# Kernel tuning notes

Hardware: AMD Instinct MI355X
Metric: run time of the kernel (lower is better)

## Reference

```python
import jax, jax.numpy as jnp
import numpy as np

TEMPERATURE = 0.07
EPS = 1e-12  # matches F.normalize eps clamp


def setup_inputs() -> dict:
    key = jax.random.key(0)
    k1, k2 = jax.random.split(key)
    B, S, D = 8, 512, 128
    return {
        "z_i": jax.random.normal(k1, (B, S, D), dtype=jnp.float32),
        "z_j": jax.random.normal(k2, (B, S, D), dtype=jnp.float32),
    }


def reference(z_i, z_j):
    D = z_i.shape[-1]
    zi = z_i.reshape(-1, D)  # [N, D]
    zj = z_j.reshape(-1, D)
    # cosine normalization (use_cosine_similarity=True)
    zi = zi / jnp.maximum(jnp.linalg.norm(zi, axis=1, keepdims=True), EPS)
    zj = zj / jnp.maximum(jnp.linalg.norm(zj, axis=1, keepdims=True), EPS)
    N = zi.shape[0]
    z = jnp.concatenate([zi, zj], axis=0)  # [2N, D]
    sim = (z @ z.T) / TEMPERATURE  # [2N, 2N]
    # denominator: logsumexp over all j != i (positives + negatives)
    diag = jnp.eye(2 * N, dtype=bool)
    lse = jax.nn.logsumexp(jnp.where(diag, -jnp.inf, sim), axis=1)  # [2N]
    # positive logit for row i is sim[i, (i+N) mod 2N] = <zi, zj>/T for both halves
    pos_half = jnp.sum(zi * zj, axis=1) / TEMPERATURE  # [N]
    pos = jnp.concatenate([pos_half, pos_half])  # [2N]
    return jnp.mean(-pos + lse)
```

## Files before the change

### kernel.cpp

```cpp
#include <hip/hip_runtime.h>
#include <stdint.h>


#define TOTAL   8192
#define NHALF   4096
#define DK      128
#define TEMP_INV 14.285714285714286f
#define SCALE    4.539816f

#define TILE    128
#define TILES   (TOTAL / TILE)
#define NBLK    (TILES * (TILES + 1) / 2)
#define BN      64
#define NSTAGE  (TILE / BN)

typedef short  bf16x8  __attribute__((ext_vector_type(8)));
typedef float  floatx4 __attribute__((ext_vector_type(4)));

#if __has_builtin(__builtin_amdgcn_exp2f)
#define EXP2(x) __builtin_amdgcn_exp2f(x)
#else
#define EXP2(x) exp2f(x)
#endif

__device__ __forceinline__ uint32_t f2bf(float f) {
  uint32_t u = __float_as_uint(f);
  return (u + 0x7fffu + ((u >> 16) & 1u)) >> 16;
}
__device__ __forceinline__ uint32_t pack2bf(float lo, float hi) {
  return f2bf(lo) | (f2bf(hi) << 16);
}

__global__ __launch_bounds__(256) void ntx_norm(
    const float* __restrict__ zi, const float* __restrict__ zj,
    uint32_t* __restrict__ zn,
    float* __restrict__ pos,
    float* __restrict__ rowsum)
{
  const int t = threadIdx.x;
  if (blockIdx.x < 32) rowsum[blockIdx.x * 256 + t] = 0.0f;

  const int wave = t >> 6, lane = t & 63;
  const int i = blockIdx.x * 4 + wave;

  const float2 vi = *(const float2*)(zi + (size_t)i * DK + lane * 2);
  const float2 vj = *(const float2*)(zj + (size_t)i * DK + lane * 2);
  float ssi = vi.x * vi.x + vi.y * vi.y;
  float ssj = vj.x * vj.x + vj.y * vj.y;
  float dij = vi.x * vj.x + vi.y * vj.y;
#pragma unroll
  for (int m = 1; m <= 32; m <<= 1) {
    ssi += __shfl_xor(ssi, m, 64);
    ssj += __shfl_xor(ssj, m, 64);
    dij += __shfl_xor(dij, m, 64);
  }
  const float invi = 1.0f / fmaxf(sqrtf(ssi), 1e-12f);
  const float invj = 1.0f / fmaxf(sqrtf(ssj), 1e-12f);

  zn[(size_t)i * 64 + lane] =
      pack2bf(vi.x * invi * SCALE, vi.y * invi * SCALE);
  zn[(size_t)(i + NHALF) * 64 + lane] =
      pack2bf(vj.x * invj * SCALE, vj.y * invj * SCALE);
  if (lane == 0) pos[i] = dij * invi * invj * TEMP_INV;
}

__global__ __launch_bounds__(128, 3) void ntx_gemm(
    const uint16_t* __restrict__ z,
    float* __restrict__ rowsum)
{
  __shared__ uint4 lb4[BN * 17];
  __shared__ float colacc[2][TILE];

  int I = 0, rem = (int)blockIdx.x, span = TILES;
  while (rem >= span) { rem -= span; --span; ++I; }
  const int J = I + rem;
  const bool isdiag = (I == J);

  const int t = threadIdx.x;
  const int wave = t >> 6, lane = t & 63;
  const int q = lane >> 4, c = lane & 15;
  const int i0 = I * TILE;
  const int j0 = J * TILE;
  const int rowbase = i0 + wave * 64;

  bf16x8 afrag[4][4];
#pragma unroll
  for (int s = 0; s < 4; ++s) {
    const uint16_t* ap = z + (size_t)(rowbase + s * 16 + c) * DK + q * 8;
#pragma unroll
    for (int kk = 0; kk < 4; ++kk)
      afrag[s][kk] = *(const bf16x8*)(ap + kk * 32);
  }

  float runsum[4][4];
#pragma unroll
  for (int s = 0; s < 4; ++s)
#pragma unroll
    for (int r = 0; r < 4; ++r) runsum[s][r] = 0.0f;

  const int ch = t & 15;
  const int r0 = t >> 4;

  for (int st = 0; st < NSTAGE; ++st) {
    const int jst = j0 + st * BN;
    __syncthreads();
#pragma unroll
    for (int p = 0; p < 8; ++p) {
      const int r = r0 + p * 8;
      uint4 v = *(const uint4*)(z + (size_t)(jst + r) * DK + ch * 8);
      lb4[r * 17 + ch] = v;
    }
    __syncthreads();

#pragma unroll
    for (int jt = 0; jt < BN / 16; ++jt) {
      bf16x8 bfrag[4];
#pragma unroll
      for (int kk = 0; kk < 4; ++kk)
        bfrag[kk] = *(const bf16x8*)&lb4[(jt * 16 + c) * 17 + kk * 4 + q];
      const int jc = jst + jt * 16;

      float colv = 0.0f;
#pragma unroll
      for (int s = 0; s < 4; ++s) {
        floatx4 acc = {0.0f, 0.0f, 0.0f, 0.0f};
#pragma unroll
        for (int kk = 0; kk < 4; ++kk)
          acc = __builtin_amdgcn_mfma_f32_16x16x32_bf16(afrag[s][kk],
                                                        bfrag[kk], acc,
                                                        0, 0, 0);
        const int rb = rowbase + s * 16;
        if (!isdiag) {
#pragma unroll
          for (int r = 0; r < 4; ++r) {
            float e = EXP2(acc[r]);
            runsum[s][r] += e;
            colv += e;
          }
        } else if (jc == rb) {
#pragma unroll
          for (int r = 0; r < 4; ++r) {
            float e = EXP2(acc[r]);
            runsum[s][r] += (q * 4 + r == c) ? 0.0f : e;
          }
        } else {
#pragma unroll
          for (int r = 0; r < 4; ++r) runsum[s][r] += EXP2(acc[r]);
        }
      }

      if (!isdiag) {
        colv += __shfl_xor(colv, 16, 64);
        colv += __shfl_xor(colv, 32, 64);
        if (lane < 16)
          colacc[wave][st * BN + jt * 16 + lane] = colv;
      }
    }
  }

#pragma unroll
  for (int s = 0; s < 4; ++s)
#pragma unroll
    for (int r = 0; r < 4; ++r) {
      float v = runsum[s][r];
      v += __shfl_xor(v, 1, 64);
      v += __shfl_xor(v, 2, 64);
      v += __shfl_xor(v, 4, 64);
      v += __shfl_xor(v, 8, 64);
      runsum[s][r] = v;
    }
  if (c == 0) {
#pragma unroll
    for (int s = 0; s < 4; ++s)
#pragma unroll
      for (int r = 0; r < 4; ++r)
        atomicAdd(&rowsum[rowbase + s * 16 + q * 4 + r], runsum[s][r]);
  }

  __syncthreads();
  if (!isdiag && t < TILE)
    atomicAdd(&rowsum[j0 + t], colacc[0][t] + colacc[1][t]);
}

__global__ __launch_bounds__(1024) void ntx_final(
    const float* __restrict__ rowsum, const float* __restrict__ pos,
    float* __restrict__ out)
{
  const int t = threadIdx.x;
  float acc = 0.0f;
  for (int r = t; r < TOTAL; r += 1024) acc += __logf(rowsum[r]);
  for (int r = t; r < NHALF; r += 1024) acc -= 2.0f * pos[r];
#pragma unroll
  for (int m = 1; m <= 32; m <<= 1) acc += __shfl_xor(acc, m, 64);
  __shared__ float red[16];
  const int wave = t >> 6, lane = t & 63;
  if (lane == 0) red[wave] = acc;
  __syncthreads();
  if (t == 0) {
    float s = 0.0f;
#pragma unroll
    for (int w = 0; w < 16; ++w) s += red[w];
    out[0] = s / (float)TOTAL;
  }
}

extern "C" void kernel_launch(void* const* d_in, const int* in_sizes, int n_in,
                              void* d_out, int out_size, void* d_ws,
                              size_t ws_size, hipStream_t stream) {
  const float* zi = (const float*)d_in[0];
  const float* zj = (const float*)d_in[1];
  float* out = (float*)d_out;

  char* ws = (char*)d_ws;
  uint16_t* zn     = (uint16_t*)ws;
  float*    rowsum = (float*)(ws + (size_t)TOTAL * DK * 2);
  float*    pos    = (float*)(ws + (size_t)TOTAL * DK * 2 + TOTAL * 4);

  ntx_norm<<<dim3(NHALF / 4), dim3(256), 0, stream>>>(zi, zj, (uint32_t*)zn,
                                                      pos, rowsum);
  ntx_gemm<<<dim3(NBLK), dim3(128), 0, stream>>>(zn, rowsum);
  ntx_final<<<dim3(1), dim3(1024), 0, stream>>>(rowsum, pos, out);
}
```

Measured before the change: 100.9 us.

## Use 4-wave GEMM blocks and replace atomics with deterministic per-block scratch reduction

```diff
diff --git a/kernel.cpp b/kernel.cpp
--- a/kernel.cpp
+++ b/kernel.cpp
@@ -34,12 +34,9 @@
 __global__ __launch_bounds__(256) void ntx_norm(
     const float* __restrict__ zi, const float* __restrict__ zj,
     uint32_t* __restrict__ zn,
-    float* __restrict__ pos,
-    float* __restrict__ rowsum)
+    float* __restrict__ pos)
 {
   const int t = threadIdx.x;
-  if (blockIdx.x < 32) rowsum[blockIdx.x * 256 + t] = 0.0f;
-
   const int wave = t >> 6, lane = t & 63;
   const int i = blockIdx.x * 4 + wave;
 
@@ -64,12 +61,12 @@
   if (lane == 0) pos[i] = dij * invi * invj * TEMP_INV;
 }
 
-__global__ __launch_bounds__(128, 3) void ntx_gemm(
+__global__ __launch_bounds__(256, 6) void ntx_gemm(
     const uint16_t* __restrict__ z,
-    float* __restrict__ rowsum)
+    float* __restrict__ scratch)
 {
   __shared__ uint4 lb4[BN * 17];
-  __shared__ float colacc[2][TILE];
+  __shared__ float colacc[4][TILE];
 
   int I = 0, rem = (int)blockIdx.x, span = TILES;
   while (rem >= span) { rem -= span; --span; ++I; }
@@ -81,20 +78,20 @@
   const int q = lane >> 4, c = lane & 15;
   const int i0 = I * TILE;
   const int j0 = J * TILE;
-  const int rowbase = i0 + wave * 64;
-
-  bf16x8 afrag[4][4];
-#pragma unroll
-  for (int s = 0; s < 4; ++s) {
+  const int rowbase = i0 + wave * 32;
+
+  bf16x8 afrag[2][4];
+#pragma unroll
+  for (int s = 0; s < 2; ++s) {
     const uint16_t* ap = z + (size_t)(rowbase + s * 16 + c) * DK + q * 8;
 #pragma unroll
     for (int kk = 0; kk < 4; ++kk)
       afrag[s][kk] = *(const bf16x8*)(ap + kk * 32);
   }
 
-  float runsum[4][4];
-#pragma unroll
-  for (int s = 0; s < 4; ++s)
+  float runsum[2][4];
+#pragma unroll
+  for (int s = 0; s < 2; ++s)
 #pragma unroll
     for (int r = 0; r < 4; ++r) runsum[s][r] = 0.0f;
 
@@ -105,8 +102,8 @@
     const int jst = j0 + st * BN;
     __syncthreads();
 #pragma unroll
-    for (int p = 0; p < 8; ++p) {
-      const int r = r0 + p * 8;
+    for (int p = 0; p < 4; ++p) {
+      const int r = r0 + p * 16;
       uint4 v = *(const uint4*)(z + (size_t)(jst + r) * DK + ch * 8);
       lb4[r * 17 + ch] = v;
     }
@@ -122,7 +119,7 @@
 
       float colv = 0.0f;
 #pragma unroll
-      for (int s = 0; s < 4; ++s) {
+      for (int s = 0; s < 2; ++s) {
         floatx4 acc = {0.0f, 0.0f, 0.0f, 0.0f};
 #pragma unroll
         for (int kk = 0; kk < 4; ++kk)
@@ -158,8 +155,9 @@
     }
   }
 
-#pragma unroll
-  for (int s = 0; s < 4; ++s)
+  float* sblk = scratch + (size_t)blockIdx.x * 256;
+#pragma unroll
+  for (int s = 0; s < 2; ++s)
 #pragma unroll
     for (int r = 0; r < 4; ++r) {
       float v = runsum[s][r];
@@ -171,37 +169,57 @@
     }
   if (c == 0) {
 #pragma unroll
-    for (int s = 0; s < 4; ++s)
+    for (int s = 0; s < 2; ++s)
 #pragma unroll
       for (int r = 0; r < 4; ++r)
-        atomicAdd(&rowsum[rowbase + s * 16 + q * 4 + r], runsum[s][r]);
+        sblk[wave * 32 + s * 16 + q * 4 + r] = runsum[s][r];
   }
 
   __syncthreads();
   if (!isdiag && t < TILE)
-    atomicAdd(&rowsum[j0 + t], colacc[0][t] + colacc[1][t]);
-}
-
-__global__ __launch_bounds__(1024) void ntx_final(
-    const float* __restrict__ rowsum, const float* __restrict__ pos,
+    sblk[128 + t] = colacc[0][t] + colacc[1][t] + colacc[2][t] + colacc[3][t];
+}
+
+__global__ __launch_bounds__(128) void ntx_redu(
+    const float* __restrict__ scratch, float* __restrict__ lpart)
+{
+  const int I = (int)blockIdx.x;
+  const int o = (int)threadIdx.x;
+
+  float S0 = 0.0f, S1 = 0.0f;
+  int id = I * TILES - (I * (I - 1)) / 2;
+#pragma unroll 4
+  for (int J = I; J < TILES; ++J, ++id)
+    S0 += scratch[(size_t)id * 256 + o];
+  int idc = I;
+#pragma unroll 4
+  for (int Ip = 0; Ip < I; ++Ip) {
+    S1 += scratch[(size_t)idc * 256 + 128 + o];
+    idc += TILES - 1 - Ip;
+  }
+
+  float v = __logf(S0 + S1);
+#pragma unroll
+  for (int m = 1; m <= 32; m <<= 1) v += __shfl_xor(v, m, 64);
+  __shared__ float red[2];
+  if ((o & 63) == 0) red[o >> 6] = v;
+  __syncthreads();
+  if (o == 0) lpart[I] = red[0] + red[1];
+}
+
+__global__ __launch_bounds__(256) void ntx_final(
+    const float* __restrict__ lpart, const float* __restrict__ pos,
     float* __restrict__ out)
 {
   const int t = threadIdx.x;
-  float acc = 0.0f;
-  for (int r = t; r < TOTAL; r += 1024) acc += __logf(rowsum[r]);
-  for (int r = t; r < NHALF; r += 1024) acc -= 2.0f * pos[r];
+  float acc = (t < TILES) ? lpart[t] : 0.0f;
+  for (int r = t; r < NHALF; r += 256) acc -= 2.0f * pos[r];
 #pragma unroll
   for (int m = 1; m <= 32; m <<= 1) acc += __shfl_xor(acc, m, 64);
-  __shared__ float red[16];
-  const int wave = t >> 6, lane = t & 63;
-  if (lane == 0) red[wave] = acc;
+  __shared__ float red[4];
+  if ((t & 63) == 0) red[t >> 6] = acc;
   __syncthreads();
-  if (t == 0) {
-    float s = 0.0f;
-#pragma unroll
-    for (int w = 0; w < 16; ++w) s += red[w];
-    out[0] = s / (float)TOTAL;
-  }
+  if (t == 0) out[0] = (red[0] + red[1] + red[2] + red[3]) / (float)TOTAL;
 }
 
 extern "C" void kernel_launch(void* const* d_in, const int* in_sizes, int n_in,
@@ -212,12 +230,16 @@
   float* out = (float*)d_out;
 
   char* ws = (char*)d_ws;
-  uint16_t* zn     = (uint16_t*)ws;
-  float*    rowsum = (float*)(ws + (size_t)TOTAL * DK * 2);
-  float*    pos    = (float*)(ws + (size_t)TOTAL * DK * 2 + TOTAL * 4);
+  uint16_t* zn      = (uint16_t*)ws;
+  float*    scratch = (float*)(ws + (size_t)TOTAL * DK * 2);
+  float*    lpart   = (float*)(ws + (size_t)TOTAL * DK * 2
+                               + (size_t)NBLK * 256 * 4);
+  float*    pos     = (float*)(ws + (size_t)TOTAL * DK * 2
+                               + (size_t)NBLK * 256 * 4 + 256);
 
   ntx_norm<<<dim3(NHALF / 4), dim3(256), 0, stream>>>(zi, zj, (uint32_t*)zn,
-                                                      pos, rowsum);
-  ntx_gemm<<<dim3(NBLK), dim3(128), 0, stream>>>(zn, rowsum);
-  ntx_final<<<dim3(1), dim3(1024), 0, stream>>>(rowsum, pos, out);
-}
+                                                      pos);
+  ntx_gemm<<<dim3(NBLK), dim3(256), 0, stream>>>(zn, scratch);
+  ntx_redu<<<dim3(TILES), dim3(128), 0, stream>>>(scratch, lpart);
+  ntx_final<<<dim3(1), dim3(256), 0, stream>>>(lpart, pos, out);
+}
```

Measured after the change: 114.4 us. +13.3%, slower.
